# Kernel tuning notes

Hardware: AMD Instinct MI355X
Metric: run time of the kernel (lower is better)

Reference implementation:

```python
import jax, jax.numpy as jnp
import numpy as np
from jax import lax

T, B, D = 128, 64, 64  # time steps, batch, embed_dim


def setup_inputs() -> dict:
    key = jax.random.key(0)
    k1, k2, k3, k4, k5 = jax.random.split(key, 5)
    scale = 1.0 / np.sqrt(D)
    return {
        "data_r": jax.random.normal(k1, (T, B, D, D), dtype=jnp.float32) * scale,
        "data_i": jax.random.normal(k2, (T, B, D, D), dtype=jnp.float32) * scale,
        "U_r": jax.random.normal(k3, (D, D), dtype=jnp.float32) * scale,
        "U_i": jax.random.normal(k4, (D, D), dtype=jnp.float32) * scale,
        "lam": jax.random.uniform(k5, (), dtype=jnp.float32),
    }


def reference(data_r, data_i, U_r, U_i, lam):
    """QRNN forward. Original loops num_layers times but every layer shares the
    same cell (ModuleList([cell]*L)) and re-consumes the raw `data`, overwriting
    in_states -- so the result equals a single-layer scan, computed here once.

    QRNNCell (reconstructed): complex density-matrix update
        v  = sigmoid(lam) * h + (1 - sigmoid(lam)) * x          (complex mix)
        h' = U v U^H                                            (unitary evolution)
    with h0 = eye(D)/D (maximally mixed state), h0_i = 0.
    """
    g = jax.nn.sigmoid(lam)
    U_rT, U_iT = U_r.T, U_i.T

    def step(h, x):
        h_r, h_i = h
        x_r, x_i = x
        # complex convex mix of hidden state and input density matrix
        v_r = g * h_r + (1.0 - g) * x_r  # [B, D, D]
        v_i = g * h_i + (1.0 - g) * x_i
        # t = U @ v   (complex):  U is [D,D], v is [B,D,D]
        t_r = jnp.einsum('pq,bqr->bpr', U_r, v_r) - jnp.einsum('pq,bqr->bpr', U_i, v_i)
        t_i = jnp.einsum('pq,bqr->bpr', U_r, v_i) + jnp.einsum('pq,bqr->bpr', U_i, v_r)
        # h' = t @ U^H, with U^H = U_r.T - i U_i.T
        hn_r = t_r @ U_rT + t_i @ U_iT
        hn_i = t_i @ U_rT - t_r @ U_iT
        return (hn_r, hn_i), (hn_r, hn_i)

    h0_r = jnp.broadcast_to(jnp.eye(D, dtype=data_r.dtype) / D, (B, D, D))
    h0_i = jnp.zeros_like(h0_r)
    _, (all_r, all_i) = lax.scan(step, (h0_r, h0_i), (data_r, data_i))
    # list of [h_r, h_i] per time step -> stacked [2, T, B, D, D]
    return jnp.stack([all_r, all_i])
```

## Files before the change

kernel.cpp:

```cpp
#include <hip/hip_runtime.h>
#include <math.h>

typedef _Float16 half8 __attribute__((ext_vector_type(8)));
typedef _Float16 half4_t __attribute__((ext_vector_type(4)));
typedef float floatx16 __attribute__((ext_vector_type(16)));
typedef float float4_t __attribute__((ext_vector_type(4)));

#define NT 128
#define NB 64
#define NC 8
#define CL 16

__device__ __forceinline__ int eidx(int row, int col) {
  return row * 64 + ((((col >> 3) ^ row) & 7) << 3) + (col & 7);
}
__device__ __forceinline__ int jcolf(int j, int pblk, int hi) {
  return 32 * pblk + (j & 3) + 8 * (j >> 2) + 4 * hi;
}

#define BARX() do {                                        \
  asm volatile("s_waitcnt lgkmcnt(0)" ::: "memory");       \
  __builtin_amdgcn_s_barrier();                            \
  __builtin_amdgcn_sched_barrier(0);                       \
} while (0)

template<bool PASS3>
__global__ __launch_bounds__(512, 2)
void qrnn_scan(const float* __restrict__ data_r, const float* __restrict__ data_i,
               const float* __restrict__ U_r, const float* __restrict__ U_i,
               const float* __restrict__ lam_p, float* __restrict__ out) {
  __shared__ __align__(16) _Float16 Vr[4096], Vi[4096];
  __shared__ __align__(16) _Float16 Tr[4096], Ti[4096];
  __shared__ __align__(16) _Float16 Xr[4096], Xi[4096];
  __shared__ __align__(16) _Float16 Or_[4096], Oi_[4096];
  __shared__ __align__(16) float red[8];

  const int bx = blockIdx.x;
  const int b  = bx & (NB - 1);
  const int c  = bx >> 6;
  const int t0 = c * CL;
  const int tid = threadIdx.x;
  const int lane = tid & 63, hi = lane >> 5, l31 = lane & 31, w = tid >> 6;
  const int grp = w >> 2, rblk = (w >> 1) & 1, pblk = w & 1;
  const int prow = 32 * rblk + l31;

  const float g = 1.0f / (1.0f + expf(-lam_p[0]));

  half8 Urh[4], Url[4], Uih[4], Uil[4];
  {
    const int row = 32 * pblk + l31;
    #pragma unroll
    for (int kq = 0; kq < 4; ++kq) {
      const int c0 = 16 * kq + 8 * hi;
      #pragma unroll
      for (int e = 0; e < 8; ++e) {
        const float ur = U_r[row * 64 + c0 + e];
        const float ui = U_i[row * 64 + c0 + e];
        _Float16 h;
        h = (_Float16)ur; Urh[kq][e] = h; Url[kq][e] = (_Float16)((ur - (float)h) * 256.0f);
        h = (_Float16)ui; Uih[kq][e] = h; Uil[kq][e] = (_Float16)((ui - (float)h) * 256.0f);
      }
    }
  }

  float rv[16];
  if constexpr (PASS3) {
    if (c == 0) {
      #pragma unroll
      for (int j = 0; j < 16; ++j)
        rv[j] = (grp == 0 && prow == jcolf(j, pblk, hi)) ? (1.0f / 64.0f) : 0.0f;
    } else {
      const float* hs = out + ((size_t)((grp ? NT : 0) + t0 + 1) * NB + b) * 4096;
      #pragma unroll
      for (int j = 0; j < 16; ++j)
        rv[j] = hs[prow * 64 + jcolf(j, pblk, hi)];
    }
  } else {
    #pragma unroll
    for (int j = 0; j < 16; ++j) rv[j] = 0.0f;
  }
  {
    float ml = 0.0f;
    #pragma unroll
    for (int j = 0; j < 16; ++j) ml = fmaxf(ml, fabsf(rv[j]));
    #pragma unroll
    for (int d = 32; d >= 1; d >>= 1) ml = fmaxf(ml, __shfl_xor(ml, d, 64));
    if (lane == 0) red[w] = ml;
  }

  const int dq = tid >> 3, dr0 = (tid & 7) * 8;
  {
    const size_t xb = ((size_t)t0 * NB + b) * 4096 + (size_t)(dq * 64 + dr0);
    float4_t a0 = *(const float4_t*)(data_r + xb);
    float4_t a1 = *(const float4_t*)(data_r + xb + 4);
    float4_t c0 = *(const float4_t*)(data_i + xb);
    float4_t c1 = *(const float4_t*)(data_i + xb + 4);
    half8 hx, hy;
    #pragma unroll
    for (int e = 0; e < 4; ++e) {
      hx[e] = (_Float16)a0[e]; hx[4 + e] = (_Float16)a1[e];
      hy[e] = (_Float16)c0[e]; hy[4 + e] = (_Float16)c1[e];
    }
    *(half8*)&Xr[eidx(dq, dr0)] = hx;
    *(half8*)&Xi[eidx(dq, dr0)] = hy;
  }
  BARX();

  float Sig, alpha = 1.0f, alphainv = 1.0f;
  {
    float4_t r0 = *(const float4_t*)&red[0];
    float4_t r1 = *(const float4_t*)&red[4];
    float mm = fmaxf(fmaxf(fmaxf(r0[0], r0[1]), fmaxf(r0[2], r0[3])),
                     fmaxf(fmaxf(r1[0], r1[1]), fmaxf(r1[2], r1[3])));
    int E0 = 0;
    if (mm > 0.0f) frexpf(mm, &E0);
    const float sc = ldexpf(1.0f, -E0);
    #pragma unroll
    for (int j = 0; j < 16; ++j) rv[j] *= sc;
    Sig = ldexpf(1.0f, E0);
  }

  for (int s = 0; s < CL; ++s) {
    {
      const float ga = g * alpha;
      const float kx = (1.0f - g) * alpha / Sig;
      const _Float16* Xg = grp ? Xi : Xr;
      _Float16* Vg = grp ? Vi : Vr;
      #pragma unroll
      for (int jj = 0; jj < 4; ++jj) {
        const int j0 = 32 * pblk + 8 * jj + 4 * hi;
        half4_t xv = *(const half4_t*)&Xg[eidx(prow, j0)];
        #pragma unroll
        for (int e = 0; e < 4; ++e) {
          const float r = rv[4 * jj + e];
          const float vv = ga * r + kx * (float)xv[e];
          Vg[eidx(j0 + e, prow)] = (_Float16)vv;
        }
      }
      if constexpr (PASS3) {
        _Float16* Og = grp ? Oi_ : Or_;
        #pragma unroll
        for (int jj = 0; jj < 4; ++jj) {
          const int j0 = 32 * pblk + 8 * jj + 4 * hi;
          half4_t ov;
          #pragma unroll
          for (int e = 0; e < 4; ++e) ov[e] = (_Float16)(alpha * rv[4 * jj + e]);
          *(half4_t*)&Og[eidx(prow, j0)] = ov;
        }
      }
      float m0[8];
      #pragma unroll
      for (int e = 0; e < 8; ++e) m0[e] = fmaxf(fabsf(rv[e]), fabsf(rv[e + 8]));
      #pragma unroll
      for (int e = 0; e < 4; ++e) m0[e] = fmaxf(m0[e], m0[e + 4]);
      float ml = fmaxf(fmaxf(m0[0], m0[1]), fmaxf(m0[2], m0[3]));
      #pragma unroll
      for (int d = 32; d >= 1; d >>= 1) ml = fmaxf(ml, __shfl_xor(ml, d, 64));
      if (lane == 0) red[w] = ml;
    }
    BARX();

    float4_t pa0, pa1, pb0, pb1;
    const bool pf = (s + 1 < CL);
    if (pf) {
      const size_t xb = ((size_t)(t0 + s + 1) * NB + b) * 4096 + (size_t)(dq * 64 + dr0);
      pa0 = *(const float4_t*)(data_r + xb);
      pa1 = *(const float4_t*)(data_r + xb + 4);
      pb0 = *(const float4_t*)(data_i + xb);
      pb1 = *(const float4_t*)(data_i + xb + 4);
    }
    Sig *= alphainv;
    if constexpr (PASS3) {
      if (s > 0) {
        half8 hr = *(const half8*)&Or_[eidx(dq, dr0)];
        half8 hm = *(const half8*)&Oi_[eidx(dq, dr0)];
        float* oR = out + ((size_t)(t0 + s - 1) * NB + b) * 4096 + (size_t)(dq * 64 + dr0);
        float4_t o0, o1, o2, o3;
        #pragma unroll
        for (int e = 0; e < 4; ++e) {
          o0[e] = Sig * (float)hr[e]; o1[e] = Sig * (float)hr[4 + e];
          o2[e] = Sig * (float)hm[e]; o3[e] = Sig * (float)hm[4 + e];
        }
        *(float4_t*)(oR) = o0;
        *(float4_t*)(oR + 4) = o1;
        *(float4_t*)(oR + (size_t)NT * NB * 4096) = o2;
        *(float4_t*)(oR + (size_t)NT * NB * 4096 + 4) = o3;
      }
    }
    {
      float4_t r0 = *(const float4_t*)&red[0];
      float4_t r1 = *(const float4_t*)&red[4];
      float mm = fmaxf(fmaxf(fmaxf(r0[0], r0[1]), fmaxf(r0[2], r0[3])),
                       fmaxf(fmaxf(r1[0], r1[1]), fmaxf(r1[2], r1[3])));
      int E = 0;
      if (mm > 0.0f) frexpf(mm, &E);
      alpha = ldexpf(1.0f, -E);
      alphainv = ldexpf(1.0f, E);
    }

    {
      half8 A0[4], A1[4];
      const int rrow = 32 * rblk + l31;
      #pragma unroll
      for (int kq = 0; kq < 4; ++kq) {
        const int cc = 16 * kq + 8 * hi;
        half8 avr = *(const half8*)&Vr[eidx(rrow, cc)];
        half8 avi = *(const half8*)&Vi[eidx(rrow, cc)];
        if (grp == 0) { A0[kq] = avr; A1[kq] = avi; }
        else          { A0[kq] = avi; A1[kq] = avr; }
      }
      floatx16 a1h, a1l, a2h, a2l;
      #pragma unroll
      for (int j = 0; j < 16; ++j) { a1h[j] = 0; a1l[j] = 0; a2h[j] = 0; a2l[j] = 0; }
      #pragma unroll
      for (int kq = 0; kq < 4; ++kq) {
        a1h = __builtin_amdgcn_mfma_f32_32x32x16_f16(A0[kq], Urh[kq], a1h, 0, 0, 0);
        a2h = __builtin_amdgcn_mfma_f32_32x32x16_f16(A1[kq], Uih[kq], a2h, 0, 0, 0);
        a1l = __builtin_amdgcn_mfma_f32_32x32x16_f16(A0[kq], Url[kq], a1l, 0, 0, 0);
        a2l = __builtin_amdgcn_mfma_f32_32x32x16_f16(A1[kq], Uil[kq], a2l, 0, 0, 0);
      }
      const float s1 = grp ? 1.0f : -1.0f;
      _Float16* Tg = grp ? Ti : Tr;
      const int tp = 32 * pblk + l31;
      #pragma unroll
      for (int jj = 0; jj < 4; ++jj) {
        const int rr0 = 32 * rblk + 8 * jj + 4 * hi;
        half4_t tv;
        #pragma unroll
        for (int e = 0; e < 4; ++e) {
          const int j = 4 * jj + e;
          tv[e] = (_Float16)((a1h[j] + s1 * a2h[j]) + (a1l[j] + s1 * a2l[j]) * 0.00390625f);
        }
        *(half4_t*)&Tg[eidx(tp, rr0)] = tv;
      }
    }
    if (pf) {
      half8 hx, hy;
      #pragma unroll
      for (int e = 0; e < 4; ++e) {
        hx[e] = (_Float16)pa0[e]; hx[4 + e] = (_Float16)pa1[e];
        hy[e] = (_Float16)pb0[e]; hy[4 + e] = (_Float16)pb1[e];
      }
      *(half8*)&Xr[eidx(dq, dr0)] = hx;
      *(half8*)&Xi[eidx(dq, dr0)] = hy;
    }
    BARX();

    {
      half8 B0[4], B1[4];
      const int p2 = 32 * rblk + l31;
      #pragma unroll
      for (int kq = 0; kq < 4; ++kq) {
        const int cc = 16 * kq + 8 * hi;
        half8 btr = *(const half8*)&Tr[eidx(p2, cc)];
        half8 bti = *(const half8*)&Ti[eidx(p2, cc)];
        if (grp == 0) { B0[kq] = btr; B1[kq] = bti; }
        else          { B0[kq] = bti; B1[kq] = btr; }
      }
      floatx16 c1h, c1l, c2h, c2l;
      #pragma unroll
      for (int j = 0; j < 16; ++j) { c1h[j] = 0; c1l[j] = 0; c2h[j] = 0; c2l[j] = 0; }
      #pragma unroll
      for (int kq = 0; kq < 4; ++kq) {
        c1h = __builtin_amdgcn_mfma_f32_32x32x16_f16(Urh[kq], B0[kq], c1h, 0, 0, 0);
        c2h = __builtin_amdgcn_mfma_f32_32x32x16_f16(Uih[kq], B1[kq], c2h, 0, 0, 0);
        c1l = __builtin_amdgcn_mfma_f32_32x32x16_f16(Url[kq], B0[kq], c1l, 0, 0, 0);
        c2l = __builtin_amdgcn_mfma_f32_32x32x16_f16(Uil[kq], B1[kq], c2l, 0, 0, 0);
      }
      const float s2 = grp ? -1.0f : 1.0f;
      #pragma unroll
      for (int j = 0; j < 16; ++j)
        rv[j] = (c1h[j] + s2 * c2h[j]) + (c1l[j] + s2 * c2l[j]) * 0.00390625f;
    }
  }

  {
    _Float16* Og = grp ? Oi_ : Or_;
    #pragma unroll
    for (int jj = 0; jj < 4; ++jj) {
      const int j0 = 32 * pblk + 8 * jj + 4 * hi;
      half4_t ov;
      #pragma unroll
      for (int e = 0; e < 4; ++e) ov[e] = (_Float16)rv[4 * jj + e];
      *(half4_t*)&Og[eidx(prow, j0)] = ov;
    }
  }
  BARX();
  {
    const int trow = PASS3 ? (t0 + CL - 1) : t0;
    float* eR = out + ((size_t)trow * NB + b) * 4096 + (size_t)(dq * 64 + dr0);
    half8 hr = *(const half8*)&Or_[eidx(dq, dr0)];
    half8 hm = *(const half8*)&Oi_[eidx(dq, dr0)];
    float4_t o0, o1, o2, o3;
    #pragma unroll
    for (int e = 0; e < 4; ++e) {
      o0[e] = Sig * (float)hr[e]; o1[e] = Sig * (float)hr[4 + e];
      o2[e] = Sig * (float)hm[e]; o3[e] = Sig * (float)hm[4 + e];
    }
    *(float4_t*)(eR) = o0;
    *(float4_t*)(eR + 4) = o1;
    *(float4_t*)(eR + (size_t)NT * NB * 4096) = o2;
    *(float4_t*)(eR + (size_t)NT * NB * 4096 + 4) = o3;
  }
}

__global__ __launch_bounds__(512, 1)
void qrnn_combine(const float* __restrict__ U_r, const float* __restrict__ U_i,
                  const float* __restrict__ lam_p, float* __restrict__ out) {
  __shared__ float Ga_r[64 * 68], Ga_i[64 * 68], Gb_r[64 * 68], Gb_i[64 * 68];
  __shared__ __align__(16) _Float16 Vr[4096], Vi[4096], Tr[4096], Ti[4096];
  __shared__ float red[8];

  const int b = blockIdx.x;
  const int tid = threadIdx.x;
  const int lane = tid & 63, hi = lane >> 5, l31 = lane & 31, w = tid >> 6;
  const int grp = w >> 2, rblk = (w >> 1) & 1, pblk = w & 1;
  const int prow = 32 * rblk + l31;

  const float g = 1.0f / (1.0f + expf(-lam_p[0]));
  const float g2 = g * g, g4 = g2 * g2, g8 = g4 * g4, g16 = g8 * g8;

  const int qr = tid >> 3, qc = (tid & 7) * 8;
  {
    *(float4_t*)&Ga_r[qr * 68 + qc]     = *(const float4_t*)(U_r + qr * 64 + qc);
    *(float4_t*)&Ga_r[qr * 68 + qc + 4] = *(const float4_t*)(U_r + qr * 64 + qc + 4);
    *(float4_t*)&Ga_i[qr * 68 + qc]     = *(const float4_t*)(U_i + qr * 64 + qc);
    *(float4_t*)&Ga_i[qr * 68 + qc + 4] = *(const float4_t*)(U_i + qr * 64 + qc + 4);
  }
  __syncthreads();

  #pragma unroll
  for (int it = 0; it < 4; ++it) {
    const float* sr = (it & 1) ? Gb_r : Ga_r;
    const float* si = (it & 1) ? Gb_i : Ga_i;
    float* dr = (it & 1) ? Ga_r : Gb_r;
    float* di = (it & 1) ? Ga_i : Gb_i;
    float cr[8], ci[8];
    #pragma unroll
    for (int e = 0; e < 8; ++e) { cr[e] = 0.0f; ci[e] = 0.0f; }
    for (int k = 0; k < 64; ++k) {
      const float ar = sr[qr * 68 + k];
      const float ai = si[qr * 68 + k];
      float4_t br0 = *(const float4_t*)&sr[k * 68 + qc];
      float4_t br1 = *(const float4_t*)&sr[k * 68 + qc + 4];
      float4_t bi0 = *(const float4_t*)&si[k * 68 + qc];
      float4_t bi1 = *(const float4_t*)&si[k * 68 + qc + 4];
      #pragma unroll
      for (int e = 0; e < 4; ++e) {
        cr[e]     += ar * br0[e] - ai * bi0[e];
        ci[e]     += ar * bi0[e] + ai * br0[e];
        cr[4 + e] += ar * br1[e] - ai * bi1[e];
        ci[4 + e] += ar * bi1[e] + ai * br1[e];
      }
    }
    float4_t s0, s1, s2, s3;
    #pragma unroll
    for (int e = 0; e < 4; ++e) { s0[e] = cr[e]; s1[e] = cr[4 + e]; s2[e] = ci[e]; s3[e] = ci[4 + e]; }
    *(float4_t*)&dr[qr * 68 + qc] = s0;  *(float4_t*)&dr[qr * 68 + qc + 4] = s1;
    *(float4_t*)&di[qr * 68 + qc] = s2;  *(float4_t*)&di[qr * 68 + qc + 4] = s3;
    __syncthreads();
  }

  half8 Wrh[4], Wrl[4], Wih[4], Wil[4];
  {
    const int row = 32 * pblk + l31;
    #pragma unroll
    for (int kq = 0; kq < 4; ++kq) {
      const int c0 = 16 * kq + 8 * hi;
      #pragma unroll
      for (int e = 0; e < 8; ++e) {
        const float wr = Ga_r[row * 68 + c0 + e];
        const float wi = Ga_i[row * 68 + c0 + e];
        _Float16 h;
        h = (_Float16)wr; Wrh[kq][e] = h; Wrl[kq][e] = (_Float16)((wr - (float)h) * 256.0f);
        h = (_Float16)wi; Wih[kq][e] = h; Wil[kq][e] = (_Float16)((wi - (float)h) * 256.0f);
      }
    }
  }

  float rv[16];
  #pragma unroll
  for (int j = 0; j < 16; ++j)
    rv[j] = (grp == 0 && prow == jcolf(j, pblk, hi)) ? (1.0f / 64.0f) : 0.0f;

  for (int c = 0; c < NC - 1; ++c) {
    float pv[16];
    {
      const float* ps = out + ((size_t)((grp ? NT : 0) + c * CL) * NB + b) * 4096;
      #pragma unroll
      for (int j = 0; j < 16; ++j) pv[j] = ps[prow * 64 + jcolf(j, pblk, hi)];
    }
    float ml = 0.0f;
    #pragma unroll
    for (int j = 0; j < 16; ++j) ml = fmaxf(ml, fabsf(rv[j]));
    #pragma unroll
    for (int d = 32; d >= 1; d >>= 1) ml = fmaxf(ml, __shfl_xor(ml, d, 64));
    if (lane == 0) red[w] = ml;
    __syncthreads();
    float mm = red[0];
    #pragma unroll
    for (int i = 1; i < 8; ++i) mm = fmaxf(mm, red[i]);
    int E = 0;
    if (mm > 0.0f) frexpf(mm, &E);
    const float al = ldexpf(1.0f, -E);
    const float fE = g16 * ldexpf(1.0f, E);

    {
      _Float16* Vg = grp ? Vi : Vr;
      #pragma unroll
      for (int j = 0; j < 16; ++j)
        Vg[eidx(jcolf(j, pblk, hi), prow)] = (_Float16)(al * rv[j]);
    }
    __syncthreads();

    {
      half8 A0[4], A1[4];
      const int rrow = 32 * rblk + l31;
      #pragma unroll
      for (int kq = 0; kq < 4; ++kq) {
        const int cc = 16 * kq + 8 * hi;
        half8 avr = *(const half8*)&Vr[eidx(rrow, cc)];
        half8 avi = *(const half8*)&Vi[eidx(rrow, cc)];
        if (grp == 0) { A0[kq] = avr; A1[kq] = avi; }
        else          { A0[kq] = avi; A1[kq] = avr; }
      }
      floatx16 a1h, a1l, a2h, a2l;
      #pragma unroll
      for (int j = 0; j < 16; ++j) { a1h[j] = 0; a1l[j] = 0; a2h[j] = 0; a2l[j] = 0; }
      #pragma unroll
      for (int kq = 0; kq < 4; ++kq) {
        a1h = __builtin_amdgcn_mfma_f32_32x32x16_f16(A0[kq], Wrh[kq], a1h, 0, 0, 0);
        a2h = __builtin_amdgcn_mfma_f32_32x32x16_f16(A1[kq], Wih[kq], a2h, 0, 0, 0);
        a1l = __builtin_amdgcn_mfma_f32_32x32x16_f16(A0[kq], Wrl[kq], a1l, 0, 0, 0);
        a2l = __builtin_amdgcn_mfma_f32_32x32x16_f16(A1[kq], Wil[kq], a2l, 0, 0, 0);
      }
      const float s1 = grp ? 1.0f : -1.0f;
      _Float16* Tg = grp ? Ti : Tr;
      const int tp = 32 * pblk + l31;
      #pragma unroll
      for (int jj = 0; jj < 4; ++jj) {
        const int rr0 = 32 * rblk + 8 * jj + 4 * hi;
        half4_t tv;
        #pragma unroll
        for (int e = 0; e < 4; ++e) {
          const int j = 4 * jj + e;
          tv[e] = (_Float16)((a1h[j] + s1 * a2h[j]) + (a1l[j] + s1 * a2l[j]) * 0.00390625f);
        }
        *(half4_t*)&Tg[eidx(tp, rr0)] = tv;
      }
    }
    __syncthreads();

    {
      half8 B0[4], B1[4];
      const int p2 = 32 * rblk + l31;
      #pragma unroll
      for (int kq = 0; kq < 4; ++kq) {
        const int cc = 16 * kq + 8 * hi;
        half8 btr = *(const half8*)&Tr[eidx(p2, cc)];
        half8 bti = *(const half8*)&Ti[eidx(p2, cc)];
        if (grp == 0) { B0[kq] = btr; B1[kq] = bti; }
        else          { B0[kq] = bti; B1[kq] = btr; }
      }
      floatx16 c1h, c1l, c2h, c2l;
      #pragma unroll
      for (int j = 0; j < 16; ++j) { c1h[j] = 0; c1l[j] = 0; c2h[j] = 0; c2l[j] = 0; }
      #pragma unroll
      for (int kq = 0; kq < 4; ++kq) {
        c1h = __builtin_amdgcn_mfma_f32_32x32x16_f16(Wrh[kq], B0[kq], c1h, 0, 0, 0);
        c2h = __builtin_amdgcn_mfma_f32_32x32x16_f16(Wih[kq], B1[kq], c2h, 0, 0, 0);
        c1l = __builtin_amdgcn_mfma_f32_32x32x16_f16(Wrl[kq], B0[kq], c1l, 0, 0, 0);
        c2l = __builtin_amdgcn_mfma_f32_32x32x16_f16(Wil[kq], B1[kq], c2l, 0, 0, 0);
      }
      const float s2 = grp ? -1.0f : 1.0f;
      #pragma unroll
      for (int j = 0; j < 16; ++j) {
        const float rvS = (c1h[j] + s2 * c2h[j]) + (c1l[j] + s2 * c2l[j]) * 0.00390625f;
        rv[j] = fE * rvS + pv[j];
      }
    }
    {
      float* hs = out + ((size_t)((grp ? NT : 0) + (c + 1) * CL + 1) * NB + b) * 4096;
      #pragma unroll
      for (int j = 0; j < 16; ++j) hs[prow * 64 + jcolf(j, pblk, hi)] = rv[j];
    }
    __syncthreads();
  }
}

extern "C" void kernel_launch(void* const* d_in, const int* in_sizes, int n_in,
                              void* d_out, int out_size, void* d_ws, size_t ws_size,
                              hipStream_t stream) {
  (void)in_sizes; (void)n_in; (void)out_size; (void)d_ws; (void)ws_size;
  const float* dr = (const float*)d_in[0];
  const float* di = (const float*)d_in[1];
  const float* ur = (const float*)d_in[2];
  const float* ui = (const float*)d_in[3];
  const float* lm = (const float*)d_in[4];
  float* o = (float*)d_out;
  qrnn_scan<false><<<dim3(NB * NC), dim3(512), 0, stream>>>(dr, di, ur, ui, lm, o);
  qrnn_combine<<<dim3(NB), dim3(512), 0, stream>>>(ur, ui, lm, o);
  qrnn_scan<true><<<dim3(NB * NC), dim3(512), 0, stream>>>(dr, di, ur, ui, lm, o);
}
```

Baseline: 299.0 us.

## Double-buffer input staging and write outputs directly from registers

New measurement: 305.3 us. 2.1% more time.

```diff
diff --git a/kernel.cpp b/kernel.cpp
--- a/kernel.cpp
+++ b/kernel.cpp
@@ -31,8 +31,7 @@
                const float* __restrict__ lam_p, float* __restrict__ out) {
   __shared__ __align__(16) _Float16 Vr[4096], Vi[4096];
   __shared__ __align__(16) _Float16 Tr[4096], Ti[4096];
-  __shared__ __align__(16) _Float16 Xr[4096], Xi[4096];
-  __shared__ __align__(16) _Float16 Or_[4096], Oi_[4096];
+  __shared__ __align__(16) _Float16 Xr[2][4096], Xi[2][4096];
   __shared__ __align__(16) float red[8];
 
   const int bx = blockIdx.x;
@@ -101,8 +100,16 @@
       hx[e] = (_Float16)a0[e]; hx[4 + e] = (_Float16)a1[e];
       hy[e] = (_Float16)c0[e]; hy[4 + e] = (_Float16)c1[e];
     }
-    *(half8*)&Xr[eidx(dq, dr0)] = hx;
-    *(half8*)&Xi[eidx(dq, dr0)] = hy;
+    *(half8*)&Xr[0][eidx(dq, dr0)] = hx;
+    *(half8*)&Xi[0][eidx(dq, dr0)] = hy;
+  }
+  float4_t pa0, pa1, pb0, pb1;
+  {
+    const size_t xb = ((size_t)(t0 + 1) * NB + b) * 4096 + (size_t)(dq * 64 + dr0);
+    pa0 = *(const float4_t*)(data_r + xb);
+    pa1 = *(const float4_t*)(data_r + xb + 4);
+    pb0 = *(const float4_t*)(data_i + xb);
+    pb1 = *(const float4_t*)(data_i + xb + 4);
   }
   BARX();
 
@@ -124,7 +131,7 @@
     {
       const float ga = g * alpha;
       const float kx = (1.0f - g) * alpha / Sig;
-      const _Float16* Xg = grp ? Xi : Xr;
+      const _Float16* Xg = grp ? Xi[s & 1] : Xr[s & 1];
       _Float16* Vg = grp ? Vi : Vr;
       #pragma unroll
       for (int jj = 0; jj < 4; ++jj) {
@@ -137,17 +144,6 @@
           Vg[eidx(j0 + e, prow)] = (_Float16)vv;
         }
       }
-      if constexpr (PASS3) {
-        _Float16* Og = grp ? Oi_ : Or_;
-        #pragma unroll
-        for (int jj = 0; jj < 4; ++jj) {
-          const int j0 = 32 * pblk + 8 * jj + 4 * hi;
-          half4_t ov;
-          #pragma unroll
-          for (int e = 0; e < 4; ++e) ov[e] = (_Float16)(alpha * rv[4 * jj + e]);
-          *(half4_t*)&Og[eidx(prow, j0)] = ov;
-        }
-      }
       float m0[8];
       #pragma unroll
       for (int e = 0; e < 8; ++e) m0[e] = fmaxf(fabsf(rv[e]), fabsf(rv[e + 8]));
@@ -160,33 +156,38 @@
     }
     BARX();
 
-    float4_t pa0, pa1, pb0, pb1;
-    const bool pf = (s + 1 < CL);
-    if (pf) {
-      const size_t xb = ((size_t)(t0 + s + 1) * NB + b) * 4096 + (size_t)(dq * 64 + dr0);
+    if (s + 1 < CL) {
+      half8 hx, hy;
+      #pragma unroll
+      for (int e = 0; e < 4; ++e) {
+        hx[e] = (_Float16)pa0[e]; hx[4 + e] = (_Float16)pa1[e];
+        hy[e] = (_Float16)pb0[e]; hy[4 + e] = (_Float16)pb1[e];
+      }
+      *(half8*)&Xr[(s + 1) & 1][eidx(dq, dr0)] = hx;
+      *(half8*)&Xi[(s + 1) & 1][eidx(dq, dr0)] = hy;
+    }
+    if (s + 2 < CL) {
+      const size_t xb = ((size_t)(t0 + s + 2) * NB + b) * 4096 + (size_t)(dq * 64 + dr0);
       pa0 = *(const float4_t*)(data_r + xb);
       pa1 = *(const float4_t*)(data_r + xb + 4);
       pb0 = *(const float4_t*)(data_i + xb);
       pb1 = *(const float4_t*)(data_i + xb + 4);
     }
-    Sig *= alphainv;
     if constexpr (PASS3) {
       if (s > 0) {
-        half8 hr = *(const half8*)&Or_[eidx(dq, dr0)];
-        half8 hm = *(const half8*)&Oi_[eidx(dq, dr0)];
-        float* oR = out + ((size_t)(t0 + s - 1) * NB + b) * 4096 + (size_t)(dq * 64 + dr0);
-        float4_t o0, o1, o2, o3;
+        float* oR = out + ((size_t)(t0 + s - 1) * NB + b) * 4096
+                        + (grp ? (size_t)NT * NB * 4096 : 0) + (size_t)(prow * 64);
         #pragma unroll
-        for (int e = 0; e < 4; ++e) {
-          o0[e] = Sig * (float)hr[e]; o1[e] = Sig * (float)hr[4 + e];
-          o2[e] = Sig * (float)hm[e]; o3[e] = Sig * (float)hm[4 + e];
+        for (int jj = 0; jj < 4; ++jj) {
+          const int j0 = 32 * pblk + 8 * jj + 4 * hi;
+          float4_t ov;
+          #pragma unroll
+          for (int e = 0; e < 4; ++e) ov[e] = Sig * rv[4 * jj + e];
+          *(float4_t*)(oR + j0) = ov;
         }
-        *(float4_t*)(oR) = o0;
-        *(float4_t*)(oR + 4) = o1;
-        *(float4_t*)(oR + (size_t)NT * NB * 4096) = o2;
-        *(float4_t*)(oR + (size_t)NT * NB * 4096 + 4) = o3;
-      }
-    }
+      }
+    }
+    Sig *= alphainv;
     {
       float4_t r0 = *(const float4_t*)&red[0];
       float4_t r1 = *(const float4_t*)&red[4];
@@ -234,16 +235,6 @@
         *(half4_t*)&Tg[eidx(tp, rr0)] = tv;
       }
     }
-    if (pf) {
-      half8 hx, hy;
-      #pragma unroll
-      for (int e = 0; e < 4; ++e) {
-        hx[e] = (_Float16)pa0[e]; hx[4 + e] = (_Float16)pa1[e];
-        hy[e] = (_Float16)pb0[e]; hy[4 + e] = (_Float16)pb1[e];
-      }
-      *(half8*)&Xr[eidx(dq, dr0)] = hx;
-      *(half8*)&Xi[eidx(dq, dr0)] = hy;
-    }
     BARX();
 
     {
@@ -275,32 +266,17 @@
   }
 
   {
-    _Float16* Og = grp ? Oi_ : Or_;
+    const int trow = PASS3 ? (t0 + CL - 1) : t0;
+    float* eR = out + ((size_t)trow * NB + b) * 4096
+                    + (grp ? (size_t)NT * NB * 4096 : 0) + (size_t)(prow * 64);
     #pragma unroll
     for (int jj = 0; jj < 4; ++jj) {
       const int j0 = 32 * pblk + 8 * jj + 4 * hi;
-      half4_t ov;
-      #pragma unroll
-      for (int e = 0; e < 4; ++e) ov[e] = (_Float16)rv[4 * jj + e];
-      *(half4_t*)&Og[eidx(prow, j0)] = ov;
-    }
-  }
-  BARX();
-  {
-    const int trow = PASS3 ? (t0 + CL - 1) : t0;
-    float* eR = out + ((size_t)trow * NB + b) * 4096 + (size_t)(dq * 64 + dr0);
-    half8 hr = *(const half8*)&Or_[eidx(dq, dr0)];
-    half8 hm = *(const half8*)&Oi_[eidx(dq, dr0)];
-    float4_t o0, o1, o2, o3;
-    #pragma unroll
-    for (int e = 0; e < 4; ++e) {
-      o0[e] = Sig * (float)hr[e]; o1[e] = Sig * (float)hr[4 + e];
-      o2[e] = Sig * (float)hm[e]; o3[e] = Sig * (float)hm[4 + e];
-    }
-    *(float4_t*)(eR) = o0;
-    *(float4_t*)(eR + 4) = o1;
-    *(float4_t*)(eR + (size_t)NT * NB * 4096) = o2;
-    *(float4_t*)(eR + (size_t)NT * NB * 4096 + 4) = o3;
+      float4_t ov;
+      #pragma unroll
+      for (int e = 0; e < 4; ++e) ov[e] = Sig * rv[4 * jj + e];
+      *(float4_t*)(eR + j0) = ov;
+    }
   }
 }
 
```
